# Performance work log

Measured on AMD Instinct MI355X. Metric: run time of the kernel, lower is better.

## Reference

```python
import jax, jax.numpy as jnp
import numpy as np

B, Q, D = 4, 1024, 1024
N, DH = 16, 64  # n_head, d_head
SCALE = 1.0 / DH ** 0.5
LN_EPS = 1e-5


def setup_inputs() -> dict:
    key = jax.random.key(0)
    ks = jax.random.split(key, 10)
    return {
        "w": jax.random.normal(ks[0], (B, Q, D), jnp.float32),
        "r_emb": jax.random.normal(ks[1], (Q, N, DH), jnp.float32),
        "r_w_bias": jax.random.normal(ks[2], (N, DH), jnp.float32),
        "r_bias": jax.random.normal(ks[3], (Q, N), jnp.float32),
        # projection weights stored [in, out]; torch Linear init std = 1/sqrt(d_head)
        "Wq": jax.random.normal(ks[4], (D, N * DH), jnp.float32) * SCALE,
        "Wk": jax.random.normal(ks[5], (D, N * DH), jnp.float32) * SCALE,
        "Wv": jax.random.normal(ks[6], (D, N * DH), jnp.float32) * SCALE,
        "Wo": jax.random.normal(ks[7], (N * DH, D), jnp.float32) * SCALE,
        "ln_gamma": jnp.ones((D,), jnp.float32),
        "ln_beta": jnp.zeros((D,), jnp.float32),
    }


def _rel_shift(x):
    # x: [b, i, j, n]; pad a zero column at the end of j then drop j=0
    # equivalent to shifting left by one along j with a trailing zero.
    return jnp.concatenate([x[:, :, 1:, :], jnp.zeros_like(x[:, :, :1, :])], axis=2)


def reference(w, r_emb, r_w_bias, r_bias, Wq, Wk, Wv, Wo, ln_gamma, ln_beta):
    b, qlen, d = w.shape
    klen = qlen  # mems=None
    n, dh = r_w_bias.shape

    q_h = (w @ Wq).reshape(b, qlen, n, dh)
    k_h = (w @ Wk).reshape(b, klen, n, dh)
    v_h = (w @ Wv).reshape(b, klen, n, dh)

    rw_q = q_h + r_w_bias[None, None]                      # [b,q,n,dh]
    AC = jnp.einsum('bind,bjnd->bijn', rw_q, k_h)          # [b,q,k,n]
    B_ = jnp.einsum('bind,jnd->bijn', q_h, r_emb)          # [b,q,k,n]
    BD = _rel_shift(B_ + r_bias[None, None])               # [b,q,k,n]

    attn_score = (AC + BD) * SCALE
    attn_prob = jax.nn.softmax(attn_score, axis=2)
    attn_vec = jnp.einsum('bijn,bjnd->bind', attn_prob, v_h)
    attn_out = attn_vec.reshape(b, qlen, n * dh) @ Wo

    out = w + attn_out  # residual (post-lnorm path)
    mu = jnp.mean(out, axis=-1, keepdims=True)
    var = jnp.var(out, axis=-1, keepdims=True)
    return (out - mu) / jnp.sqrt(var + LN_EPS) * ln_gamma + ln_beta
```

## Files before the change

kernel.cpp:

```cpp
#include <hip/hip_runtime.h>
#include <hip/hip_bf16.h>

using f16 = _Float16;
typedef _Float16 f16x8 __attribute__((ext_vector_type(8)));
typedef _Float16 f16x4 __attribute__((ext_vector_type(4)));
typedef float f32x4 __attribute__((ext_vector_type(4)));

#define AS1 __attribute__((address_space(1)))
#define AS3 __attribute__((address_space(3)))

constexpr int Bc = 4, Qc = 1024, Dc = 1024, Nh = 16, DHc = 64;
constexpr int BQ = Bc * Qc;
constexpr int NHEAD = Bc * Nh;
constexpr float ATT_SCALE = 0.125f;

__global__ void k_f2h(const float* __restrict__ src, f16* __restrict__ dst) {
    long i8 = ((long)blockIdx.x * blockDim.x + threadIdx.x) * 8;
    float4 a = *(const float4*)&src[i8];
    float4 b = *(const float4*)&src[i8 + 4];
    f16x8 o = { (f16)a.x, (f16)a.y, (f16)a.z, (f16)a.w,
                (f16)b.x, (f16)b.y, (f16)b.z, (f16)b.w };
    *(f16x8*)&dst[i8] = o;
}

struct Ptr4 { const float* p[4]; };
__global__ void k_transpose4(Ptr4 srcs, f16* __restrict__ dst) {
    __shared__ f16 tile[32][33];
    const float* src = srcs.p[blockIdx.z];
    f16* d = dst + (long)blockIdx.z * Dc * Dc;
    int c0 = blockIdx.x * 32, r0 = blockIdx.y * 32;
#pragma unroll
    for (int dy = 0; dy < 32; dy += 8) {
        int r = r0 + threadIdx.y + dy, c = c0 + threadIdx.x;
        tile[threadIdx.y + dy][threadIdx.x] = (f16)src[(long)r * Dc + c];
    }
    __syncthreads();
#pragma unroll
    for (int dy = 0; dy < 32; dy += 8) {
        int c = c0 + threadIdx.y + dy, r = r0 + threadIdx.x;
        d[(long)c * Dc + r] = tile[threadIdx.x][threadIdx.y + dy];
    }
}

__global__ void k_fill_remb(const float* __restrict__ remb, f16* __restrict__ Kt) {
    long gid = (long)blockIdx.x * blockDim.x + threadIdx.x;
    int d8 = (int)(gid & 7) * 8;
    int j = (int)((gid >> 3) & 1023);
    int h = (int)(gid >> 13);
    int n = h & 15;
    f16x8 kv;
    if (j < 1023) {
        const float* rp = &remb[((long)(j + 1) * 16 + n) * 64 + d8];
        float4 r0 = *(const float4*)rp, r1 = *(const float4*)(rp + 4);
        kv[0] = (f16)r0.x; kv[1] = (f16)r0.y; kv[2] = (f16)r0.z; kv[3] = (f16)r0.w;
        kv[4] = (f16)r1.x; kv[5] = (f16)r1.y; kv[6] = (f16)r1.z; kv[7] = (f16)r1.w;
    } else {
        kv = f16x8{};
    }
    *(f16x8*)&Kt[(((long)h << 10) + j) * 128 + 64 + d8] = kv;
}

template <int BM, int BN, int BK, int WROWS, int WCOLS, int EPI>
__global__ __launch_bounds__(256) void k_gemm_nt(
    const f16* __restrict__ A, const f16* __restrict__ Bt, void* __restrict__ Cv,
    const float* __restrict__ aux, f16* __restrict__ qtp, f16* __restrict__ ktp,
    f16* __restrict__ vtp, int lda, int ldb, int ldc, int K)
{
    constexpr int TM = BM / (WROWS * 16);
    constexpr int TN = BN / (WCOLS * 16);
    __shared__ __align__(16) f16 sA[BM * BK];
    __shared__ __align__(16) f16 sB[BN * BK];

    const int tid = threadIdx.x;
    const int lane = tid & 63, wave = tid >> 6;
    const int wm = wave / WCOLS, wn = wave % WCOLS;
    const int m0 = blockIdx.y * BM, n0 = blockIdx.x * BN;

    f32x4 acc[TM][TN] = {};

    const int lrow = lane & 15;
    const int kq = (lane >> 4) * 8;
    const int srow = lane >> 2;
    const int scol = (lane & 3) * 8;

    for (int k0 = 0; k0 < K; k0 += BK) {
        __syncthreads();
        constexpr int CHA = BM * BK / 512;
#pragma unroll
        for (int ch = 0; ch < CHA / 4; ++ch) {
            int cc = ch * 4 + wave;
            __builtin_amdgcn_global_load_lds(
                (const AS1 void*)(const void*)&A[(long)(m0 + cc * 16 + srow) * lda + k0 + scol],
                (AS3 void*)(void*)&sA[cc * 512], 16, 0, 0);
        }
        constexpr int CHB = BN * BK / 512;
#pragma unroll
        for (int ch = 0; ch < CHB / 4; ++ch) {
            int cc = ch * 4 + wave;
            __builtin_amdgcn_global_load_lds(
                (const AS1 void*)(const void*)&Bt[(long)(n0 + cc * 16 + srow) * ldb + k0 + scol],
                (AS3 void*)(void*)&sB[cc * 512], 16, 0, 0);
        }
        __syncthreads();

        f16x8 af[TM], bfr[TN];
#pragma unroll
        for (int mi = 0; mi < TM; ++mi)
            af[mi] = *(const f16x8*)&sA[(wm * TM * 16 + mi * 16 + lrow) * BK + kq];
#pragma unroll
        for (int ni = 0; ni < TN; ++ni)
            bfr[ni] = *(const f16x8*)&sB[(wn * TN * 16 + ni * 16 + lrow) * BK + kq];
#pragma unroll
        for (int mi = 0; mi < TM; ++mi)
#pragma unroll
            for (int ni = 0; ni < TN; ++ni)
                acc[mi][ni] = __builtin_amdgcn_mfma_f32_16x16x32_f16(af[mi], bfr[ni], acc[mi][ni], 0, 0, 0);
    }

    const int crow = (lane >> 4) * 4;
    const int ccol = lane & 15;
#pragma unroll
    for (int mi = 0; mi < TM; ++mi)
#pragma unroll
        for (int ni = 0; ni < TN; ++ni)
#pragma unroll
            for (int r = 0; r < 4; ++r) {
                int gm = m0 + wm * TM * 16 + mi * 16 + crow + r;
                int gn = n0 + wn * TN * 16 + ni * 16 + ccol;
                float val = acc[mi][ni][r];
                if constexpr (EPI == 1) {
                    ((float*)Cv)[(long)gm * ldc + gn] = val;
                } else {
                    int seg = n0 >> 10;
                    int col = gn & 1023;
                    int n = col >> 6, d = col & 63, b = gm >> 10, i = gm & 1023;
                    long rowbase = ((((long)((b << 4) + n) << 10) + i) << 7);
                    if (seg == 0) {
                        qtp[rowbase + d] = (f16)(val + aux[col]);
                        qtp[rowbase + 64 + d] = (f16)val;
                    } else if (seg == 1) {
                        ktp[rowbase + d] = (f16)val;
                    } else {
                        vtp[(((long)(b << 10) + col) << 10) + i] = (f16)val;
                    }
                }
            }
}

__global__ __launch_bounds__(256, 2) void k_flash(
    const f16* __restrict__ Qt, const f16* __restrict__ Kt,
    const f16* __restrict__ vT, const float* __restrict__ r_bias,
    f16* __restrict__ avp)
{
    constexpr int LDL = 136;
    __shared__ __align__(16) f16 sK[128 * LDL];
    __shared__ __align__(16) f16 sV[64 * LDL];
    __shared__ float sRB[128];

    const int tid = threadIdx.x, lane = tid & 63, wave = tid >> 6;
    const int i0 = blockIdx.x * 128;
    const int h = blockIdx.y;
    const int b = h >> 4, n = h & 15;

    const f16* Qh = Qt + (long)h * Qc * 128;
    const f16* Kh = Kt + (long)h * Qc * 128;
    const f16* Vh = vT + (long)h * DHc * Qc;

    const int lrow = lane & 15;
    const int quad = lane >> 4;
    const int kq = quad * 8;

    f16x8 aq[2][4];
#pragma unroll
    for (int t = 0; t < 2; ++t)
#pragma unroll
        for (int kc = 0; kc < 4; ++kc)
            aq[t][kc] = *(const f16x8*)&Qh[(long)(i0 + wave * 32 + t * 16 + lrow) * 128 + kc * 32 + kq];

    float m_i[2] = {-1e30f, -1e30f}, l_i[2] = {0.0f, 0.0f};
    f32x4 o_acc[2][4] = {};

    for (int j0 = 0; j0 < Qc; j0 += 128) {
        __syncthreads();
        for (int idx = tid; idx < 128 * 16; idx += 256) {
            int r = idx >> 4, c = (idx & 15) * 8;
            *(uint4*)&sK[r * LDL + c] = *(const uint4*)&Kh[(long)(j0 + r) * 128 + c];
        }
        for (int idx = tid; idx < 64 * 16; idx += 256) {
            int r = idx >> 4, c = (idx & 15) * 8;
            *(uint4*)&sV[r * LDL + c] = *(const uint4*)&Vh[(long)r * Qc + j0 + c];
        }
        if (tid < 128) {
            int j = j0 + tid;
            sRB[tid] = (j < Qc - 1) ? r_bias[(j + 1) * Nh + n] : 0.0f;
        }
        __syncthreads();

        f32x4 s_acc[2][8] = {};
#pragma unroll
        for (int kc = 0; kc < 4; ++kc)
#pragma unroll
            for (int ni = 0; ni < 8; ++ni) {
                f16x8 bk = *(const f16x8*)&sK[(ni * 16 + lrow) * LDL + kc * 32 + kq];
                s_acc[0][ni] = __builtin_amdgcn_mfma_f32_16x16x32_f16(bk, aq[0][kc], s_acc[0][ni], 0, 0, 0);
                s_acc[1][ni] = __builtin_amdgcn_mfma_f32_16x16x32_f16(bk, aq[1][kc], s_acc[1][ni], 0, 0, 0);
            }

        f16x4 pf[2][8];
        float alpha_t[2];
#pragma unroll
        for (int t = 0; t < 2; ++t) {
            float mx = -1e30f;
#pragma unroll
            for (int ni = 0; ni < 8; ++ni) {
                f32x4 rb4 = *(const f32x4*)&sRB[ni * 16 + quad * 4];
#pragma unroll
                for (int r = 0; r < 4; ++r) {
                    float v = (s_acc[t][ni][r] + rb4[r]) * ATT_SCALE;
                    s_acc[t][ni][r] = v;
                    mx = fmaxf(mx, v);
                }
            }
            mx = fmaxf(mx, __shfl_xor(mx, 16));
            mx = fmaxf(mx, __shfl_xor(mx, 32));
            float mn = fmaxf(m_i[t], mx);
            float alpha = __expf(m_i[t] - mn);
            float sm = 0.0f;
#pragma unroll
            for (int ni = 0; ni < 8; ++ni) {
                float e0 = __expf(s_acc[t][ni][0] - mn);
                float e1 = __expf(s_acc[t][ni][1] - mn);
                float e2 = __expf(s_acc[t][ni][2] - mn);
                float e3 = __expf(s_acc[t][ni][3] - mn);
                sm += (e0 + e1) + (e2 + e3);
                f16x4 pv; pv[0] = (f16)e0; pv[1] = (f16)e1; pv[2] = (f16)e2; pv[3] = (f16)e3;
                pf[t][ni] = pv;
            }
            sm += __shfl_xor(sm, 16);
            sm += __shfl_xor(sm, 32);
            l_i[t] = l_i[t] * alpha + sm;
            m_i[t] = mn;
            alpha_t[t] = alpha;
        }

#pragma unroll
        for (int t = 0; t < 2; ++t)
#pragma unroll
            for (int r = 0; r < 4; ++r) {
                float al = __shfl(alpha_t[t], quad * 4 + r);
#pragma unroll
                for (int dt = 0; dt < 4; ++dt) o_acc[t][dt][r] *= al;
            }

#pragma unroll
        for (int nj = 0; nj < 8; ++nj)
#pragma unroll
            for (int dt = 0; dt < 4; ++dt) {
                f16x4 bv = *(const f16x4*)&sV[(dt * 16 + lrow) * LDL + nj * 16 + quad * 4];
                o_acc[0][dt] = __builtin_amdgcn_mfma_f32_16x16x16f16(pf[0][nj], bv, o_acc[0][dt], 0, 0, 0);
                o_acc[1][dt] = __builtin_amdgcn_mfma_f32_16x16x16f16(pf[1][nj], bv, o_acc[1][dt], 0, 0, 0);
            }
    }

#pragma unroll
    for (int t = 0; t < 2; ++t) {
        float linv = 1.0f / l_i[t];
#pragma unroll
        for (int r = 0; r < 4; ++r) {
            float li = __shfl(linv, quad * 4 + r);
            int i = i0 + wave * 32 + t * 16 + quad * 4 + r;
#pragma unroll
            for (int dt = 0; dt < 4; ++dt) {
                int d = dt * 16 + lrow;
                avp[((long)(b * Qc + i) << 10) + n * 64 + d] = (f16)(o_acc[t][dt][r] * li);
            }
        }
    }
}

__global__ __launch_bounds__(256) void k_res_ln(const float* __restrict__ w, const float* __restrict__ ao,
                                                const float* __restrict__ gamma, const float* __restrict__ beta,
                                                float* __restrict__ out) {
    const long base = (long)blockIdx.x * 1024;
    const int tid = threadIdx.x;
    float x[4], s = 0.0f, s2 = 0.0f;
#pragma unroll
    for (int k = 0; k < 4; ++k) {
        int j = tid + k * 256;
        x[k] = w[base + j] + ao[base + j];
        s += x[k];
        s2 += x[k] * x[k];
    }
#pragma unroll
    for (int off = 32; off; off >>= 1) { s += __shfl_down(s, off); s2 += __shfl_down(s2, off); }
    __shared__ float rs[4], rs2[4];
    if ((tid & 63) == 0) { rs[tid >> 6] = s; rs2[tid >> 6] = s2; }
    __syncthreads();
    s = rs[0] + rs[1] + rs[2] + rs[3];
    s2 = rs2[0] + rs2[1] + rs2[2] + rs2[3];
    float mu = s * (1.0f / 1024.0f);
    float var = s2 * (1.0f / 1024.0f) - mu * mu;
    float inv = rsqrtf(var + 1e-5f);
#pragma unroll
    for (int k = 0; k < 4; ++k) {
        int j = tid + k * 256;
        out[base + j] = (x[k] - mu) * inv * gamma[j] + beta[j];
    }
}

extern "C" void kernel_launch(void* const* d_in, const int* in_sizes, int n_in,
                              void* d_out, int out_size, void* d_ws, size_t ws_size,
                              hipStream_t stream) {
    const float* w_in   = (const float*)d_in[0];
    const float* r_emb  = (const float*)d_in[1];
    const float* r_wb   = (const float*)d_in[2];
    const float* r_bias = (const float*)d_in[3];
    const float* Wq     = (const float*)d_in[4];
    const float* Wk     = (const float*)d_in[5];
    const float* Wv     = (const float*)d_in[6];
    const float* Wo     = (const float*)d_in[7];
    const float* ln_g   = (const float*)d_in[8];
    const float* ln_b   = (const float*)d_in[9];
    float* out = (float*)d_out;

    char* p = (char*)d_ws;
    auto alloc = [&](size_t bytes) { char* r = p; p += (bytes + 255) & ~(size_t)255; return r; };
    f16* wh = (f16*)alloc((size_t)BQ * Dc * 2);
    f16* WT = (f16*)alloc((size_t)4 * Dc * Dc * 2);
    f16* Qt = (f16*)alloc((size_t)NHEAD * Qc * 128 * 2);
    f16* Kt = (f16*)alloc((size_t)NHEAD * Qc * 128 * 2);
    f16* vT = (f16*)alloc((size_t)BQ * Dc * 2);
    f16* WoT = WT + (size_t)3 * Dc * Dc;
    f16*   avp = wh;
    float* ao  = (float*)Qt;

    k_f2h<<<(BQ * Dc) / (256 * 8), 256, 0, stream>>>(w_in, wh);

    Ptr4 srcs{{Wq, Wk, Wv, Wo}};
    k_transpose4<<<dim3(32, 32, 4), dim3(32, 8), 0, stream>>>(srcs, WT);

    k_fill_remb<<<(NHEAD * Qc * 8) / 256, 256, 0, stream>>>(r_emb, Kt);

    k_gemm_nt<128, 128, 32, 2, 2, 5><<<dim3(3 * Dc / 128, BQ / 128), 256, 0, stream>>>(
        wh, WT, nullptr, r_wb, Qt, Kt, vT, Dc, Dc, 0, Dc);

    k_flash<<<dim3(Qc / 128, NHEAD), 256, 0, stream>>>(Qt, Kt, vT, r_bias, avp);

    k_gemm_nt<64, 128, 32, 2, 2, 1><<<dim3(Dc / 128, BQ / 64), 256, 0, stream>>>(
        avp, WoT, ao, nullptr, nullptr, nullptr, nullptr, Dc, Dc, Dc, Dc);

    k_res_ln<<<BQ, 256, 0, stream>>>(w_in, ao, ln_g, ln_b, out);
}
```

Baseline: 241.4 us.

## Prefetch flash K/V tiles in registers, remap blocks, write fp16 attention output

The flash kernel now loads the next K/V/bias tile into registers while computing on the current one, then stores it to shared memory at the next iteration. Block indices are flattened and remapped so consecutive blocks cover different heads at the same query tile. The output projection GEMM now writes fp16 instead of fp32, and the residual+LayerNorm kernel reads it with vectorised float4/f16x4 accesses. These changes aim to hide global load latency and cut memory traffic, at the cost of more registers in the flash kernel and reduced precision of the attention output.

```diff
diff --git a/kernel.cpp b/kernel.cpp
--- a/kernel.cpp
+++ b/kernel.cpp
@@ -128,8 +128,8 @@
                 int gm = m0 + wm * TM * 16 + mi * 16 + crow + r;
                 int gn = n0 + wn * TN * 16 + ni * 16 + ccol;
                 float val = acc[mi][ni][r];
-                if constexpr (EPI == 1) {
-                    ((float*)Cv)[(long)gm * ldc + gn] = val;
+                if constexpr (EPI == 0) {
+                    ((f16*)Cv)[(long)gm * ldc + gn] = (f16)val;
                 } else {
                     int seg = n0 >> 10;
                     int col = gn & 1023;
@@ -158,8 +158,9 @@
     __shared__ float sRB[128];
 
     const int tid = threadIdx.x, lane = tid & 63, wave = tid >> 6;
-    const int i0 = blockIdx.x * 128;
-    const int h = blockIdx.y;
+    const int bid = blockIdx.x;
+    const int h = (((bid >> 3) & 7) << 3) | (bid & 7);
+    const int i0 = (bid >> 6) * 128;
     const int b = h >> 4, n = h & 15;
 
     const f16* Qh = Qt + (long)h * Qc * 128;
@@ -180,21 +181,41 @@
     float m_i[2] = {-1e30f, -1e30f}, l_i[2] = {0.0f, 0.0f};
     f32x4 o_acc[2][4] = {};
 
+    f16x8 pk[8], pv[4];
+    float prb;
+    auto load_tile = [&](int j0) {
+#pragma unroll
+        for (int s = 0; s < 8; ++s) {
+            int slot = s * 256 + tid, r = slot >> 4, c = (slot & 15) * 8;
+            pk[s] = *(const f16x8*)&Kh[(long)(j0 + r) * 128 + c];
+        }
+#pragma unroll
+        for (int s = 0; s < 4; ++s) {
+            int slot = s * 256 + tid, r = slot >> 4, c = (slot & 15) * 8;
+            pv[s] = *(const f16x8*)&Vh[(long)r * Qc + j0 + c];
+        }
+        int j = j0 + tid;
+        prb = (tid < 128 && j < Qc - 1) ? r_bias[(j + 1) * Nh + n] : 0.0f;
+    };
+
+    load_tile(0);
+
     for (int j0 = 0; j0 < Qc; j0 += 128) {
         __syncthreads();
-        for (int idx = tid; idx < 128 * 16; idx += 256) {
-            int r = idx >> 4, c = (idx & 15) * 8;
-            *(uint4*)&sK[r * LDL + c] = *(const uint4*)&Kh[(long)(j0 + r) * 128 + c];
-        }
-        for (int idx = tid; idx < 64 * 16; idx += 256) {
-            int r = idx >> 4, c = (idx & 15) * 8;
-            *(uint4*)&sV[r * LDL + c] = *(const uint4*)&Vh[(long)r * Qc + j0 + c];
-        }
-        if (tid < 128) {
-            int j = j0 + tid;
-            sRB[tid] = (j < Qc - 1) ? r_bias[(j + 1) * Nh + n] : 0.0f;
-        }
+#pragma unroll
+        for (int s = 0; s < 8; ++s) {
+            int slot = s * 256 + tid, r = slot >> 4, c = (slot & 15) * 8;
+            *(f16x8*)&sK[r * LDL + c] = pk[s];
+        }
+#pragma unroll
+        for (int s = 0; s < 4; ++s) {
+            int slot = s * 256 + tid, r = slot >> 4, c = (slot & 15) * 8;
+            *(f16x8*)&sV[r * LDL + c] = pv[s];
+        }
+        if (tid < 128) sRB[tid] = prb;
         __syncthreads();
+
+        if (j0 + 128 < Qc) load_tile(j0 + 128);
 
         f32x4 s_acc[2][8] = {};
 #pragma unroll
@@ -233,8 +254,8 @@
                 float e2 = __expf(s_acc[t][ni][2] - mn);
                 float e3 = __expf(s_acc[t][ni][3] - mn);
                 sm += (e0 + e1) + (e2 + e3);
-                f16x4 pv; pv[0] = (f16)e0; pv[1] = (f16)e1; pv[2] = (f16)e2; pv[3] = (f16)e3;
-                pf[t][ni] = pv;
+                f16x4 pvv; pvv[0] = (f16)e0; pvv[1] = (f16)e1; pvv[2] = (f16)e2; pvv[3] = (f16)e3;
+                pf[t][ni] = pvv;
             }
             sm += __shfl_xor(sm, 16);
             sm += __shfl_xor(sm, 32);
@@ -278,19 +299,17 @@
     }
 }
 
-__global__ __launch_bounds__(256) void k_res_ln(const float* __restrict__ w, const float* __restrict__ ao,
+__global__ __launch_bounds__(256) void k_res_ln(const float* __restrict__ w, const f16* __restrict__ ao,
                                                 const float* __restrict__ gamma, const float* __restrict__ beta,
                                                 float* __restrict__ out) {
     const long base = (long)blockIdx.x * 1024;
     const int tid = threadIdx.x;
-    float x[4], s = 0.0f, s2 = 0.0f;
-#pragma unroll
-    for (int k = 0; k < 4; ++k) {
-        int j = tid + k * 256;
-        x[k] = w[base + j] + ao[base + j];
-        s += x[k];
-        s2 += x[k] * x[k];
-    }
+    float4 wv = *(const float4*)&w[base + tid * 4];
+    f16x4 av = *(const f16x4*)&ao[base + tid * 4];
+    float x[4] = { wv.x + (float)av[0], wv.y + (float)av[1],
+                   wv.z + (float)av[2], wv.w + (float)av[3] };
+    float s = x[0] + x[1] + x[2] + x[3];
+    float s2 = x[0] * x[0] + x[1] * x[1] + x[2] * x[2] + x[3] * x[3];
 #pragma unroll
     for (int off = 32; off; off >>= 1) { s += __shfl_down(s, off); s2 += __shfl_down(s2, off); }
     __shared__ float rs[4], rs2[4];
@@ -301,11 +320,14 @@
     float mu = s * (1.0f / 1024.0f);
     float var = s2 * (1.0f / 1024.0f) - mu * mu;
     float inv = rsqrtf(var + 1e-5f);
-#pragma unroll
-    for (int k = 0; k < 4; ++k) {
-        int j = tid + k * 256;
-        out[base + j] = (x[k] - mu) * inv * gamma[j] + beta[j];
-    }
+    float4 gv = *(const float4*)&gamma[tid * 4];
+    float4 bv = *(const float4*)&beta[tid * 4];
+    float4 o;
+    o.x = (x[0] - mu) * inv * gv.x + bv.x;
+    o.y = (x[1] - mu) * inv * gv.y + bv.y;
+    o.z = (x[2] - mu) * inv * gv.z + bv.z;
+    o.w = (x[3] - mu) * inv * gv.w + bv.w;
+    *(float4*)&out[base + tid * 4] = o;
 }
 
 extern "C" void kernel_launch(void* const* d_in, const int* in_sizes, int n_in,
@@ -331,8 +353,8 @@
     f16* Kt = (f16*)alloc((size_t)NHEAD * Qc * 128 * 2);
     f16* vT = (f16*)alloc((size_t)BQ * Dc * 2);
     f16* WoT = WT + (size_t)3 * Dc * Dc;
-    f16*   avp = wh;
-    float* ao  = (float*)Qt;
+    f16* avp = wh;
+    f16* ao  = (f16*)Qt;
 
     k_f2h<<<(BQ * Dc) / (256 * 8), 256, 0, stream>>>(w_in, wh);
 
@@ -344,9 +366,9 @@
     k_gemm_nt<128, 128, 32, 2, 2, 5><<<dim3(3 * Dc / 128, BQ / 128), 256, 0, stream>>>(
         wh, WT, nullptr, r_wb, Qt, Kt, vT, Dc, Dc, 0, Dc);
 
-    k_flash<<<dim3(Qc / 128, NHEAD), 256, 0, stream>>>(Qt, Kt, vT, r_bias, avp);
-
-    k_gemm_nt<64, 128, 32, 2, 2, 1><<<dim3(Dc / 128, BQ / 64), 256, 0, stream>>>(
+    k_flash<<<512, 256, 0, stream>>>(Qt, Kt, vT, r_bias, avp);
+
+    k_gemm_nt<64, 128, 32, 2, 2, 0><<<dim3(Dc / 128, BQ / 64), 256, 0, stream>>>(
         avp, WoT, ao, nullptr, nullptr, nullptr, nullptr, Dc, Dc, Dc, Dc);
 
     k_res_ln<<<BQ, 256, 0, stream>>>(w_in, ao, ln_g, ln_b, out);
```

After: 286.4 us. 1.19x slower.
